# Performance work log

Hardware: AMD Instinct MI355X
Metric: run time of the kernel (lower is better)

Reference implementation:

```python
import jax, jax.numpy as jnp
import numpy as np

EPS = 1e-5

def conv1d(x, w, b, stride, pad):
    # x: [N, Cin, L], w: [Cout, Cin, K]
    out = jax.lax.conv_general_dilated(x, w, (stride,), [(pad, pad)], dimension_numbers=('NCH', 'OIH', 'NCH'))
    return out + b[None, :, None]

def bn_eval(x, g, b):
    # BatchNorm1d in eval mode with running_mean=0, running_var=1
    return x * (g / jnp.sqrt(1.0 + EPS))[None, :, None] + b[None, :, None]

def maxpool3(x):
    return jax.lax.reduce_window(x, -jnp.inf, jax.lax.max, (1, 1, 3), (1, 1, 3), 'VALID')

def layer_norm(x, g, b):
    m = x.mean(-1, keepdims=True)
    v = ((x - m) ** 2).mean(-1, keepdims=True)
    return (x - m) / jnp.sqrt(v + EPS) * g + b

def lstm_dir(x, w_ih, w_hh, b_ih, b_hh, reverse):
    # x: [B, S, I]; torch gate order i, f, g, o
    B = x.shape[0]; H = w_hh.shape[1]
    xs = jnp.einsum('bsi,gi->bsg', x, w_ih) + b_ih + b_hh
    if reverse:
        xs = xs[:, ::-1]
    def step(carry, xt):
        h, c = carry
        gates = xt + h @ w_hh.T
        i, f, g, o = jnp.split(gates, 4, axis=-1)
        c = jax.nn.sigmoid(f) * c + jax.nn.sigmoid(i) * jnp.tanh(g)
        h = jax.nn.sigmoid(o) * jnp.tanh(c)
        return (h, c), h
    init = (jnp.zeros((B, H), x.dtype), jnp.zeros((B, H), x.dtype))
    _, hs = jax.lax.scan(step, init, jnp.swapaxes(xs, 0, 1))
    hs = jnp.swapaxes(hs, 0, 1)
    return hs[:, ::-1] if reverse else hs

def setup_inputs() -> dict:
    key = jax.random.key(0)
    ks = iter(jax.random.split(key, 48))
    def rn(shape, s=0.05):
        return jax.random.normal(next(ks), shape, jnp.float32) * s
    B, S, C, T, F0, Hg, Hl, NC = 64, 20, 8, 3000, 64, 128, 256, 5
    return dict(
        x=jax.random.normal(next(ks), (B, S, C, T), jnp.float32),
        edge_index=jax.random.randint(next(ks), (2, 56), 0, C, jnp.int32),
        conv1_w=rn((16, 1, 7)), conv1_b=jnp.zeros(16), bn1_g=jnp.ones(16), bn1_b=jnp.zeros(16),
        conv2_w=rn((32, 16, 5)), conv2_b=jnp.zeros(32), bn2_g=jnp.ones(32), bn2_b=jnp.zeros(32),
        conv3_w=rn((F0, 32, 3)), conv3_b=jnp.zeros(F0), bn3_g=jnp.ones(F0), bn3_b=jnp.zeros(F0),
        gcn0_w=rn((Hg, F0)), gcn0_b=jnp.zeros(Hg),
        gcn1_w=rn((Hg, Hg)), gcn1_b=jnp.zeros(Hg),
        gnn_ln_g=jnp.ones(Hg), gnn_ln_b=jnp.zeros(Hg),
        w_ih_l0=rn((4 * Hl, Hg)), w_hh_l0=rn((4 * Hl, Hl)), b_ih_l0=jnp.zeros(4 * Hl), b_hh_l0=jnp.zeros(4 * Hl),
        w_ih_l0r=rn((4 * Hl, Hg)), w_hh_l0r=rn((4 * Hl, Hl)), b_ih_l0r=jnp.zeros(4 * Hl), b_hh_l0r=jnp.zeros(4 * Hl),
        w_ih_l1=rn((4 * Hl, 2 * Hl)), w_hh_l1=rn((4 * Hl, Hl)), b_ih_l1=jnp.zeros(4 * Hl), b_hh_l1=jnp.zeros(4 * Hl),
        w_ih_l1r=rn((4 * Hl, 2 * Hl)), w_hh_l1r=rn((4 * Hl, Hl)), b_ih_l1r=jnp.zeros(4 * Hl), b_hh_l1r=jnp.zeros(4 * Hl),
        lstm_ln_g=jnp.ones(2 * Hl), lstm_ln_b=jnp.zeros(2 * Hl),
        cls_w=rn((NC, 2 * Hl)), cls_b=jnp.zeros(NC),
    )

def reference(x, edge_index, conv1_w, conv1_b, bn1_g, bn1_b, conv2_w, conv2_b, bn2_g, bn2_b, conv3_w, conv3_b, bn3_g, bn3_b, gcn0_w, gcn0_b, gcn1_w, gcn1_b, gnn_ln_g, gnn_ln_b, w_ih_l0, w_hh_l0, b_ih_l0, b_hh_l0, w_ih_l0r, w_hh_l0r, b_ih_l0r, b_hh_l0r, w_ih_l1, w_hh_l1, b_ih_l1, b_hh_l1, w_ih_l1r, w_hh_l1r, b_ih_l1r, b_hh_l1r, lstm_ln_g, lstm_ln_b, cls_w, cls_b):
    B, S, C, T = x.shape
    # batched per-channel CNN over all B*S epochs at once (original: python double loop)
    h = x.reshape(B * S * C, 1, T)
    h = maxpool3(jax.nn.relu(bn_eval(conv1d(h, conv1_w, conv1_b, 2, 3), bn1_g, bn1_b)))
    h = maxpool3(jax.nn.relu(bn_eval(conv1d(h, conv2_w, conv2_b, 2, 2), bn2_g, bn2_b)))
    h = jax.nn.relu(bn_eval(conv1d(h, conv3_w, conv3_b, 1, 1), bn3_g, bn3_b))
    feats = h.mean(-1).reshape(B * S, C, -1)  # AdaptiveAvgPool1d(1) -> [BS, C, 64]
    # GCNConv normalized adjacency: D^-1/2 (A + I) D^-1/2, graph is tiny (C nodes) so dense is exact and efficient
    src, dst = edge_index[0], edge_index[1]
    A = jnp.zeros((C, C), x.dtype).at[dst, src].add(1.0) + jnp.eye(C, dtype=x.dtype)
    dinv = 1.0 / jnp.sqrt(A.sum(1))
    An = A * dinv[:, None] * dinv[None, :]
    g1 = jax.nn.relu(jnp.einsum('ij,bjf->bif', An, feats @ gcn0_w.T) + gcn0_b)  # dropout off (eval)
    g2 = jnp.einsum('ij,bjf->bif', An, g1 @ gcn1_w.T) + gcn1_b
    g2 = layer_norm(g2, gnn_ln_g, gnn_ln_b)
    emb = g2.mean(1).reshape(B, S, -1)  # mean over nodes -> [B, S, 128]
    l0 = jnp.concatenate([lstm_dir(emb, w_ih_l0, w_hh_l0, b_ih_l0, b_hh_l0, False),
                          lstm_dir(emb, w_ih_l0r, w_hh_l0r, b_ih_l0r, b_hh_l0r, True)], -1)
    l1 = jnp.concatenate([lstm_dir(l0, w_ih_l1, w_hh_l1, b_ih_l1, b_hh_l1, False),
                          lstm_dir(l0, w_ih_l1r, w_hh_l1r, b_ih_l1r, b_hh_l1r, True)], -1)
    out = layer_norm(l1, lstm_ln_g, lstm_ln_b)
    return out @ cls_w.T + cls_b  # [B, S, 5]
```

## Files before the change

### kernel.cpp

```cpp
#include <hip/hip_runtime.h>
#include <hip/hip_bf16.h>

#define DEVI __device__ __forceinline__

typedef _Float16 h2f16 __attribute__((ext_vector_type(2)));
typedef _Float16 f16x4 __attribute__((ext_vector_type(4)));
typedef _Float16 f16x8 __attribute__((ext_vector_type(8)));
typedef float    f32x4 __attribute__((ext_vector_type(4)));
union U4H { uint4 u; h2f16 h[4]; };
union F8  { f16x8 v8; f16x4 v4[2]; };

DEVI float sigf(float x){ return 1.f/(1.f + __expf(-x)); }
DEVI float tanh_f(float x){
  float ax = fabsf(x);
  float e = __expf(-2.f*ax);
  float t = (1.f - e)/(1.f + e);
  return copysignf(t, x);
}
DEVI h2f16 hmax2(h2f16 a, h2f16 b){
  h2f16 r; r[0] = a[0] > b[0] ? a[0] : b[0]; r[1] = a[1] > b[1] ? a[1] : b[1]; return r;
}

__global__ __launch_bounds__(256) void k_prep(
  const int* __restrict__ ei, float* __restrict__ An,
  const float* __restrict__ w2, const float* __restrict__ w3,
  const float* __restrict__ bg2, const float* __restrict__ bg3,
  _Float16* __restrict__ bw2f, _Float16* __restrict__ bw3f,
  const float* __restrict__ a0, const float* __restrict__ a1,
  const float* __restrict__ a2, const float* __restrict__ a3,
  const float* __restrict__ a4, const float* __restrict__ a5,
  _Float16* __restrict__ o0, _Float16* __restrict__ o1,
  _Float16* __restrict__ o2, _Float16* __restrict__ o3,
  _Float16* __restrict__ o4, _Float16* __restrict__ o5,
  const float* __restrict__ whh0, const float* __restrict__ whh0r,
  const float* __restrict__ whh1, const float* __restrict__ whh1r,
  h2f16* __restrict__ wt0f, h2f16* __restrict__ wt0r,
  h2f16* __restrict__ wt1f, h2f16* __restrict__ wt1r)
{
  const int bid = blockIdx.x, tid = threadIdx.x;
  if (bid == 0){
    __shared__ float A[64];
    __shared__ float dinv[8];
    if (tid<64) A[tid] = ((tid>>3)==(tid&7)) ? 1.f : 0.f;
    __syncthreads();
    if (tid==0){
      for (int e=0;e<56;e++){ int s=ei[e], d=ei[56+e]; A[d*8+s] += 1.f; }
    }
    __syncthreads();
    if (tid<8){ float s=0.f; for (int j=0;j<8;j++) s+=A[tid*8+j]; dinv[tid]=rsqrtf(s); }
    __syncthreads();
    if (tid<64) An[tid] = A[tid]*dinv[tid>>3]*dinv[tid&7];
    return;
  }
  if (bid <= 24){
    const int i = (bid-1)*256 + tid;
    const float rs = rsqrtf(1.f+1e-5f);
    if (i < 3072){
      const int j = i&7, m = (i>>3)&15, g = (i>>7)&3, nt = (i>>9)&1, s = i>>10;
      const int kk = 32*s + 8*g + j;
      const int k = kk >> 4, ic = kk & 15, oc = nt*16 + m;
      bw2f[i] = (_Float16)((k < 5 ? w2[oc*80 + ic*5 + k] : 0.f) * (bg2[oc]*rs));
    }
    if (i < 6144){
      const int j = i&7, m = (i>>3)&15, g = (i>>7)&3, wv = (i>>9)&3, s = i>>11;
      const int kk = 32*s + 8*g + j;
      const int k = kk >> 5, ic = kk & 31, oc = wv*16 + m;
      bw3f[i] = (_Float16)(w3[oc*96 + ic*3 + k] * (bg3[oc]*rs));
    }
    return;
  }
  if (bid <= 5240){
    const int i = (bid-25)*256 + tid;
    if      (i <  131072) o0[i] = (_Float16)a0[i];
    else if (i <  262144) o1[i-131072] = (_Float16)a1[i-131072];
    else if (i <  786432) o2[i-262144] = (_Float16)a2[i-262144];
    else if (i < 1310720) o3[i-786432] = (_Float16)a3[i-786432];
    else if (i < 1318912) o4[i-1310720] = (_Float16)a4[i-1310720];
    else if (i < 1335296) o5[i-1318912] = (_Float16)a5[i-1318912];
    return;
  }
  {
    const int idx = (bid-5241)*256 + tid;
    const int which = idx >> 17, i = idx & 131071;
    const int g = i & 1023, jp = i >> 10;
    const float* in = (which==0) ? whh0 : (which==1) ? whh0r : (which==2) ? whh1 : whh1r;
    h2f16* outp    = (which==0) ? wt0f : (which==1) ? wt0r  : (which==2) ? wt1f : wt1r;
    h2f16 p;
    p[0] = (_Float16)in[g*256 + 2*jp];
    p[1] = (_Float16)in[g*256 + 2*jp + 1];
    outp[(long)jp*1024 + g] = p;
  }
}

__global__ __launch_bounds__(512,8) void k_conv(
    const float* __restrict__ x,
    const float* __restrict__ w1g, const float* __restrict__ c1b,
    const float* __restrict__ bg1, const float* __restrict__ bb1,
    const _Float16* __restrict__ bw2f,
    const float* __restrict__ c2b, const float* __restrict__ bg2, const float* __restrict__ bb2,
    const _Float16* __restrict__ bw3f,
    const float* __restrict__ c3b, const float* __restrict__ bg3, const float* __restrict__ bb3,
    _Float16* __restrict__ feats)
{
  __shared__ __align__(16) unsigned char smb[38592];
  __shared__ h2f16 w1p[16][4];
  __shared__ float kb1o[16], kb2o[32], kb3o[64];
  __shared__ float redc[8][16];
  h2f16* sxh = reinterpret_cast<h2f16*>(smb + 20160);
  const int tid = threadIdx.x;
  const long sig = blockIdx.x;
  const float* xg = x + sig*3000;

  {
    const float4* xg4 = reinterpret_cast<const float4*>(xg);
    for (int i=tid; i<750; i+=512){
      float4 v = xg4[i];
      h2f16 p0; p0[0]=(_Float16)v.x; p0[1]=(_Float16)v.y;
      h2f16 p1; p1[0]=(_Float16)v.z; p1[1]=(_Float16)v.w;
      sxh[2*i+2] = p0; sxh[2*i+3] = p1;
    }
    if (tid<3){
      h2f16 z; z[0]=(_Float16)0.f; z[1]=(_Float16)0.f;
      sxh[tid<2 ? tid : 1502] = z;
    }
    if (tid<32){
      const int rr = tid>>3, cp = tid&7;
      const int row = (rr<2) ? rr : (500+rr);
      h2f16 z; z[0]=(_Float16)0.f; z[1]=(_Float16)0.f;
      *reinterpret_cast<h2f16*>(smb + row*40 + 4*cp) = z;
    }
    const float rs = rsqrtf(1.f+1e-5f);
    if (tid<64){
      const int c = tid>>2, j = tid&3;
      const float s = bg1[c]*rs;
      h2f16 p;
      if (j==0){ p[0]=(_Float16)0.f; p[1]=(_Float16)(w1g[c*7+0]*s); }
      else     { p[0]=(_Float16)(w1g[c*7+2*j-1]*s); p[1]=(_Float16)(w1g[c*7+2*j]*s); }
      w1p[c][j] = p;
    }
    if (tid<16) kb1o[tid] = c1b[tid]*(bg1[tid]*rs) + bb1[tid];
    if (tid<32) kb2o[tid] = c2b[tid]*(bg2[tid]*rs) + bb2[tid];
    if (tid<64) kb3o[tid] = c3b[tid]*(bg3[tid]*rs) + bb3[tid];
  }
  __syncthreads();

  {
    const int cp = tid & 7;
    h2f16 wpa[4], wpb[4];
    #pragma unroll
    for (int j=0;j<4;j++){ wpa[j] = w1p[2*cp][j]; wpb[j] = w1p[2*cp+1][j]; }
    const float oa = kb1o[2*cp], ob = kb1o[2*cp+1];
    for (int u = tid>>3; u<500; u+=64){
      h2f16 xq[6];
      #pragma unroll
      for (int r=0;r<6;r++) xq[r] = sxh[3*u + r];
      float a0=0.f,a1=0.f,a2=0.f,b0=0.f,b1=0.f,b2=0.f;
      #pragma unroll
      for (int j=0;j<4;j++){
        a0 = __builtin_amdgcn_fdot2(xq[j],   wpa[j], a0, false);
        a1 = __builtin_amdgcn_fdot2(xq[j+1], wpa[j], a1, false);
        a2 = __builtin_amdgcn_fdot2(xq[j+2], wpa[j], a2, false);
        b0 = __builtin_amdgcn_fdot2(xq[j],   wpb[j], b0, false);
        b1 = __builtin_amdgcn_fdot2(xq[j+1], wpb[j], b1, false);
        b2 = __builtin_amdgcn_fdot2(xq[j+2], wpb[j], b2, false);
      }
      const float ya = fmaxf(fmaxf(fmaxf(a0,a1),a2) + oa, 0.f);
      const float yb = fmaxf(fmaxf(fmaxf(b0,b1),b2) + ob, 0.f);
      h2f16 p; p[0]=(_Float16)ya; p[1]=(_Float16)yb;
      *reinterpret_cast<h2f16*>(smb + (u+2)*40 + 4*cp) = p;
    }
  }
  __syncthreads();

  const int wv = tid >> 6, lane = tid & 63;
  const int m = lane & 15, g = lane >> 4;

  {
    const int nt = wv & 1;
    f16x8 bf[3];
    #pragma unroll
    for (int s=0;s<3;s++)
      bf[s] = *reinterpret_cast<const f16x8*>(&bw2f[(((s*2+nt)*4+g)*16+m)*8]);
    const int oc = nt*16 + m;
    const float of = kb2o[oc];
    #pragma unroll
    for (int i=0;i<4;i++){
      const int mt = (wv>>1) + 4*i;
      const int trow = mt*16 + m;
      f32x4 acc = {0.f,0.f,0.f,0.f};
      #pragma unroll
      for (int s=0;s<3;s++){
        const int kk = 32*s + 8*g;
        const int k = kk >> 4;
        const int ab = 80*trow + 40*k + 16*(g&1);
        F8 a;
        a.v4[0] = *reinterpret_cast<const f16x4*>(smb + ab);
        a.v4[1] = *reinterpret_cast<const f16x4*>(smb + ab + 8);
        acc = __builtin_amdgcn_mfma_f32_16x16x32_f16(a.v8, bf[s], acc, 0,0,0);
      }
      #pragma unroll
      for (int r=0;r<4;r++){
        const int t = mt*16 + 4*g + r;
        const float z = fmaxf(acc[r] + of, 0.f);
        *reinterpret_cast<_Float16*>(smb + 20160 + t*72 + 2*oc) = (_Float16)z;
      }
    }
  }
  __syncthreads();

  {
    if (tid < 240){
      const int rr = tid >> 4, cc = tid & 15;
      const int row = (rr == 0) ? 0 : (83 + rr);
      h2f16 z; z[0]=(_Float16)0.f; z[1]=(_Float16)0.f;
      *reinterpret_cast<h2f16*>(smb + row*80 + 4*cc) = z;
    }
    for (int i=tid; i<1328; i+=512){
      const int u = i >> 4, cc = i & 15;
      h2f16 a = *reinterpret_cast<const h2f16*>(smb + 20160 + (3*u)*72 + 4*cc);
      h2f16 b = *reinterpret_cast<const h2f16*>(smb + 20160 + (3*u+1)*72 + 4*cc);
      h2f16 c = *reinterpret_cast<const h2f16*>(smb + 20160 + (3*u+2)*72 + 4*cc);
      *reinterpret_cast<h2f16*>(smb + (u+1)*80 + 4*cc) = hmax2(hmax2(a,b), c);
    }
  }
  __syncthreads();

  {
    const int nt = wv & 3;
    f16x8 bf[3];
    #pragma unroll
    for (int s=0;s<3;s++)
      bf[s] = *reinterpret_cast<const f16x8*>(&bw3f[(((s*4+nt)*4+g)*16+m)*8]);
    const int oc = nt*16 + m;
    const float of = kb3o[oc];
    float macc = 0.f;
    #pragma unroll
    for (int q=0;q<3;q++){
      const int mt = (wv>>2) + 2*q;
      const int trow = mt*16 + m;
      f32x4 acc = {0.f,0.f,0.f,0.f};
      #pragma unroll
      for (int s=0;s<3;s++){
        f16x8 af = *reinterpret_cast<const f16x8*>(smb + (trow + s)*80 + 16*g);
        acc = __builtin_amdgcn_mfma_f32_16x16x32_f16(af, bf[s], acc, 0,0,0);
      }
      #pragma unroll
      for (int r=0;r<4;r++){
        const int t = mt*16 + 4*g + r;
        if (t < 83) macc += fmaxf(acc[r] + of, 0.f);
      }
    }
    macc += __shfl_xor(macc, 16);
    macc += __shfl_xor(macc, 32);
    if (lane < 16) redc[wv][m] = macc;
  }
  __syncthreads();
  if (tid < 64)
    feats[sig*64 + tid] = (_Float16)((redc[tid>>4][tid&15] + redc[(tid>>4)+4][tid&15]) * (1.f/83.f));
}

__global__ __launch_bounds__(256) void k_gemm_mf(
  const _Float16* __restrict__ X, const _Float16* __restrict__ W,
  const float* __restrict__ b1, const float* __restrict__ b2,
  float* __restrict__ C, int M, int N, int K, int ldc)
{
  __shared__ __align__(16) unsigned char lds[128*72];
  unsigned char* Xs = lds;
  unsigned char* Ws = lds + 64*72;
  const int tid = threadIdx.x;
  const int m0 = blockIdx.y*64, n0 = blockIdx.x*64;
  const int wv = tid>>6, lane = tid&63, m = lane&15, g = lane>>4;
  const int sr = tid>>2, sq = tid&3;
  f32x4 acc[4] = {{0.f,0.f,0.f,0.f},{0.f,0.f,0.f,0.f},{0.f,0.f,0.f,0.f},{0.f,0.f,0.f,0.f}};
  for (int k0=0; k0<K; k0+=32){
    uint4 xa = *reinterpret_cast<const uint4*>(X + (long)(m0+sr)*K + k0 + sq*8);
    uint4 wa = *reinterpret_cast<const uint4*>(W + (long)(n0+sr)*K + k0 + sq*8);
    __syncthreads();
    *reinterpret_cast<uint4*>(Xs + sr*72 + sq*16) = xa;
    *reinterpret_cast<uint4*>(Ws + sr*72 + sq*16) = wa;
    __syncthreads();
    f16x8 af = *reinterpret_cast<const f16x8*>(Xs + (wv*16+m)*72 + g*16);
    #pragma unroll
    for (int nt=0;nt<4;nt++){
      f16x8 bf = *reinterpret_cast<const f16x8*>(Ws + (nt*16+m)*72 + g*16);
      acc[nt] = __builtin_amdgcn_mfma_f32_16x16x32_f16(af, bf, acc[nt], 0,0,0);
    }
  }
  #pragma unroll
  for (int nt=0;nt<4;nt++){
    const int col = n0 + nt*16 + m;
    float bias = 0.f;
    if (b1) bias += b1[col];
    if (b2) bias += b2[col];
    #pragma unroll
    for (int r=0;r<4;r++)
      C[(long)(m0 + wv*16 + g*4 + r)*ldc + col] = acc[nt][r] + bias;
  }
}

__global__ __launch_bounds__(256) void k_gemm_mf2(
  const _Float16* __restrict__ X,
  const _Float16* __restrict__ Wa, const _Float16* __restrict__ Wb,
  const float* __restrict__ b1a, const float* __restrict__ b2a,
  const float* __restrict__ b1b, const float* __restrict__ b2b,
  float* __restrict__ C, int co, int M, int N, int K, int ldc)
{
  __shared__ __align__(16) unsigned char lds[128*72];
  unsigned char* Xs = lds;
  unsigned char* Ws = lds + 64*72;
  const int z = blockIdx.z;
  const _Float16* W = z ? Wb : Wa;
  const float* b1 = z ? b1b : b1a;
  const float* b2 = z ? b2b : b2a;
  float* Cz = C + (z ? co : 0);
  const int tid = threadIdx.x;
  const int m0 = blockIdx.y*64, n0 = blockIdx.x*64;
  const int wv = tid>>6, lane = tid&63, m = lane&15, g = lane>>4;
  const int sr = tid>>2, sq = tid&3;
  f32x4 acc[4] = {{0.f,0.f,0.f,0.f},{0.f,0.f,0.f,0.f},{0.f,0.f,0.f,0.f},{0.f,0.f,0.f,0.f}};
  for (int k0=0; k0<K; k0+=32){
    uint4 xa = *reinterpret_cast<const uint4*>(X + (long)(m0+sr)*K + k0 + sq*8);
    uint4 wa = *reinterpret_cast<const uint4*>(W + (long)(n0+sr)*K + k0 + sq*8);
    __syncthreads();
    *reinterpret_cast<uint4*>(Xs + sr*72 + sq*16) = xa;
    *reinterpret_cast<uint4*>(Ws + sr*72 + sq*16) = wa;
    __syncthreads();
    f16x8 af = *reinterpret_cast<const f16x8*>(Xs + (wv*16+m)*72 + g*16);
    #pragma unroll
    for (int nt=0;nt<4;nt++){
      f16x8 bf = *reinterpret_cast<const f16x8*>(Ws + (nt*16+m)*72 + g*16);
      acc[nt] = __builtin_amdgcn_mfma_f32_16x16x32_f16(af, bf, acc[nt], 0,0,0);
    }
  }
  #pragma unroll
  for (int nt=0;nt<4;nt++){
    const int col = n0 + nt*16 + m;
    float bias = b1[col] + b2[col];
    #pragma unroll
    for (int r=0;r<4;r++)
      Cz[(long)(m0 + wv*16 + g*4 + r)*ldc + col] = acc[nt][r] + bias;
  }
}

__global__ __launch_bounds__(256) void k_mix1(
  const float* __restrict__ tmp0, const float* __restrict__ An,
  const float* __restrict__ b0, _Float16* __restrict__ g1)
{
  __shared__ float ans[64];
  if (threadIdx.x < 64) ans[threadIdx.x] = An[threadIdx.x];
  __syncthreads();
  const long idx = (long)blockIdx.x*256 + threadIdx.x;
  const int g = (int)(idx >> 7), j = (int)(idx & 127);
  const float* base = tmp0 + (long)g*1024;
  float t[8];
  #pragma unroll
  for (int c=0;c<8;c++) t[c] = base[c*128+j];
  const float bj = b0[j];
  #pragma unroll
  for (int i=0;i<8;i++){
    float s = bj;
    #pragma unroll
    for (int c=0;c<8;c++) s += ans[i*8+c]*t[c];
    g1[(long)g*1024 + i*128 + j] = (_Float16)fmaxf(s, 0.f);
  }
}

__global__ __launch_bounds__(128) void k_mix2(
  const float* __restrict__ tmp1, const float* __restrict__ An,
  const float* __restrict__ b1, const float* __restrict__ lng,
  const float* __restrict__ lnb, _Float16* __restrict__ emb)
{
  const int g = blockIdx.x, j = threadIdx.x;
  __shared__ float ans[64];
  __shared__ float g2s[8*128];
  __shared__ float stats[16];
  if (j<64) ans[j] = An[j];
  const float* base = tmp1 + (long)g*1024;
  float t[8];
  #pragma unroll
  for (int c=0;c<8;c++) t[c] = base[c*128 + j];
  const float bj = b1[j];
  __syncthreads();
  #pragma unroll
  for (int i=0;i<8;i++){
    float s = bj;
    #pragma unroll
    for (int c=0;c<8;c++) s += ans[i*8+c]*t[c];
    g2s[i*128+j] = s;
  }
  __syncthreads();
  {
    const int c = j>>4, l = j&15;
    float s=0.f, sq=0.f;
    for (int jj=l; jj<128; jj+=16){ float v=g2s[c*128+jj]; s+=v; sq+=v*v; }
    #pragma unroll
    for (int off=8; off>=1; off>>=1){ s += __shfl_xor(s, off); sq += __shfl_xor(sq, off); }
    if (l==0){
      float m = s*(1.f/128.f);
      stats[2*c] = m;
      stats[2*c+1] = rsqrtf(sq*(1.f/128.f) - m*m + 1e-5f);
    }
  }
  __syncthreads();
  float acc=0.f;
  #pragma unroll
  for (int i=0;i<8;i++) acc += (g2s[i*128+j] - stats[2*i]) * stats[2*i+1];
  emb[(long)g*128 + j] = (_Float16)(lng[j]*acc*0.125f + lnb[j]);
}

__global__ __launch_bounds__(1024) void k_lstm(
    const float* __restrict__ xs,
    const h2f16* __restrict__ wtf,
    const h2f16* __restrict__ wtr,
    float* __restrict__ outf,
    _Float16* __restrict__ outh)
{
  const int S = 20;
  const int b = blockIdx.x >> 1, dir = blockIdx.x & 1;
  const h2f16* wt = dir ? wtr : wtf;
  __shared__ float part[4][1024];
  __shared__ _Float16 hsh[256];
  __shared__ __align__(16) unsigned char wlds[98304];
  const int tid = threadIdx.x;
  const int jg = tid >> 8, r = tid & 255, grow = r*4;
  uint4 wreg[20];
  #pragma unroll
  for (int jp=0;jp<20;jp++)
    wreg[jp] = *reinterpret_cast<const uint4*>(
        reinterpret_cast<const unsigned int*>(wt + (long)(jg*32+jp)*1024 + grow));
  {
    const uint4* wsrc = reinterpret_cast<const uint4*>(wt);
    uint4* wdst = reinterpret_cast<uint4*>(wlds);
    for (int i=tid; i<6144; i+=1024){
      const int src = (i < 3072) ? (5120 + i) : (13312 + (i - 3072));
      wdst[i] = wsrc[src];
    }
  }
  if (tid < 256) hsh[tid] = (_Float16)0.f;
  float cc = 0.f;
  __syncthreads();
  const h2f16* hp2 = reinterpret_cast<const h2f16*>(hsh);
  for (int st=0; st<S; ++st){
    const int t = dir ? (S-1-st) : st;
    float a0=0.f,a1=0.f,a2=0.f,a3=0.f;
    #pragma unroll
    for (int jp=0; jp<20; ++jp){
      const h2f16 hv = hp2[jg*32 + jp];
      U4H w; w.u = wreg[jp];
      a0 = __builtin_amdgcn_fdot2(hv, w.h[0], a0, false);
      a1 = __builtin_amdgcn_fdot2(hv, w.h[1], a1, false);
      a2 = __builtin_amdgcn_fdot2(hv, w.h[2], a2, false);
      a3 = __builtin_amdgcn_fdot2(hv, w.h[3], a3, false);
    }
    if (jg < 2){
      #pragma unroll 6
      for (int jp=20; jp<32; ++jp){
        const h2f16 hv = hp2[jg*32 + jp];
        U4H w; w.u = *reinterpret_cast<const uint4*>(
            wlds + (long)(jg*12 + (jp-20))*4096 + grow*4);
        a0 = __builtin_amdgcn_fdot2(hv, w.h[0], a0, false);
        a1 = __builtin_amdgcn_fdot2(hv, w.h[1], a1, false);
        a2 = __builtin_amdgcn_fdot2(hv, w.h[2], a2, false);
        a3 = __builtin_amdgcn_fdot2(hv, w.h[3], a3, false);
      }
    } else {
      #pragma unroll 6
      for (int jp=20; jp<32; ++jp){
        const h2f16 hv = hp2[jg*32 + jp];
        U4H w; w.u = *reinterpret_cast<const uint4*>(
            reinterpret_cast<const unsigned int*>(wt + (long)(jg*32+jp)*1024 + grow));
        a0 = __builtin_amdgcn_fdot2(hv, w.h[0], a0, false);
        a1 = __builtin_amdgcn_fdot2(hv, w.h[1], a1, false);
        a2 = __builtin_amdgcn_fdot2(hv, w.h[2], a2, false);
        a3 = __builtin_amdgcn_fdot2(hv, w.h[3], a3, false);
      }
    }
    *reinterpret_cast<float4*>(&part[jg][grow]) = make_float4(a0,a1,a2,a3);
    __syncthreads();
    if (tid < 256){
      const float* xrow = xs + ((long)b*S + t)*2048 + dir*1024;
      float g0 = xrow[tid]
               + (part[0][tid]      + part[1][tid])      + (part[2][tid]      + part[3][tid]);
      float g1 = xrow[256+tid]
               + (part[0][256+tid]  + part[1][256+tid])  + (part[2][256+tid]  + part[3][256+tid]);
      float g2 = xrow[512+tid]
               + (part[0][512+tid]  + part[1][512+tid])  + (part[2][512+tid]  + part[3][512+tid]);
      float g3 = xrow[768+tid]
               + (part[0][768+tid]  + part[1][768+tid])  + (part[2][768+tid]  + part[3][768+tid]);
      cc = sigf(g1)*cc + sigf(g0)*tanh_f(g2);
      const float h = sigf(g3)*tanh_f(cc);
      hsh[tid] = (_Float16)h;
      const long o = ((long)b*S + t)*512 + dir*256 + tid;
      if (outf) outf[o] = h;
      if (outh) outh[o] = (_Float16)h;
    }
    __syncthreads();
  }
}

__global__ __launch_bounds__(128) void k_lncls(
  const float* __restrict__ in, const float* __restrict__ g,
  const float* __restrict__ b, const float* __restrict__ cw,
  const float* __restrict__ cb, float* __restrict__ out)
{
  const int row = blockIdx.x, tid = threadIdx.x;
  __shared__ float sred[4];
  __shared__ float cred[2][5];
  float4 v = *reinterpret_cast<const float4*>(in + (long)row*512 + tid*4);
  float s  = v.x+v.y+v.z+v.w;
  float sq = v.x*v.x+v.y*v.y+v.z*v.z+v.w*v.w;
  #pragma unroll
  for (int off=32; off>=1; off>>=1){ s += __shfl_xor(s, off); sq += __shfl_xor(sq, off); }
  const int wv = tid>>6;
  if ((tid&63)==0){ sred[wv*2]=s; sred[wv*2+1]=sq; }
  __syncthreads();
  const float S = sred[0]+sred[2], SQ = sred[1]+sred[3];
  const float m = S*(1.f/512.f);
  const float rstd = rsqrtf(SQ*(1.f/512.f) - m*m + 1e-5f);
  float4 gg = *reinterpret_cast<const float4*>(g + tid*4);
  float4 bb = *reinterpret_cast<const float4*>(b + tid*4);
  const float n0 = (v.x-m)*rstd*gg.x + bb.x;
  const float n1 = (v.y-m)*rstd*gg.y + bb.y;
  const float n2 = (v.z-m)*rstd*gg.z + bb.z;
  const float n3 = (v.w-m)*rstd*gg.w + bb.w;
  #pragma unroll
  for (int nc=0; nc<5; ++nc){
    float4 w = *reinterpret_cast<const float4*>(cw + nc*512 + tid*4);
    float p = n0*w.x + n1*w.y + n2*w.z + n3*w.w;
    #pragma unroll
    for (int off=32; off>=1; off>>=1) p += __shfl_xor(p, off);
    if ((tid&63)==0) cred[wv][nc] = p;
  }
  __syncthreads();
  if (tid < 5) out[(long)row*5 + tid] = cred[0][tid] + cred[1][tid] + cb[tid];
}

extern "C" void kernel_launch(void* const* d_in, const int* in_sizes, int n_in,
                              void* d_out, int out_size, void* d_ws, size_t ws_size,
                              hipStream_t stream)
{
  const float* x     = (const float*)d_in[0];
  const int*   ei    = (const int*)d_in[1];
  const float* w1    = (const float*)d_in[2];
  const float* c1b   = (const float*)d_in[3];
  const float* bg1   = (const float*)d_in[4];
  const float* bb1   = (const float*)d_in[5];
  const float* w2    = (const float*)d_in[6];
  const float* c2b   = (const float*)d_in[7];
  const float* bg2   = (const float*)d_in[8];
  const float* bb2   = (const float*)d_in[9];
  const float* w3    = (const float*)d_in[10];
  const float* c3b   = (const float*)d_in[11];
  const float* bg3   = (const float*)d_in[12];
  const float* bb3   = (const float*)d_in[13];
  const float* gcn0w = (const float*)d_in[14];
  const float* gcn0b = (const float*)d_in[15];
  const float* gcn1w = (const float*)d_in[16];
  const float* gcn1b = (const float*)d_in[17];
  const float* lng   = (const float*)d_in[18];
  const float* lnb   = (const float*)d_in[19];
  const float* wih0  = (const float*)d_in[20];
  const float* whh0  = (const float*)d_in[21];
  const float* bih0  = (const float*)d_in[22];
  const float* bhh0  = (const float*)d_in[23];
  const float* wih0r = (const float*)d_in[24];
  const float* whh0r = (const float*)d_in[25];
  const float* bih0r = (const float*)d_in[26];
  const float* bhh0r = (const float*)d_in[27];
  const float* wih1  = (const float*)d_in[28];
  const float* whh1  = (const float*)d_in[29];
  const float* bih1  = (const float*)d_in[30];
  const float* bhh1  = (const float*)d_in[31];
  const float* wih1r = (const float*)d_in[32];
  const float* whh1r = (const float*)d_in[33];
  const float* bih1r = (const float*)d_in[34];
  const float* bhh1r = (const float*)d_in[35];
  const float* lstmg = (const float*)d_in[36];
  const float* lstmb = (const float*)d_in[37];
  const float* clsw  = (const float*)d_in[38];
  const float* clsb  = (const float*)d_in[39];
  float* ws  = (float*)d_ws;
  float* out = (float*)d_out;

  float*    An      = ws + 0;
  _Float16* bw2f    = (_Float16*)(ws + 64);
  _Float16* bw3f    = (_Float16*)(ws + 1600);
  _Float16* feats16 = (_Float16*)(ws + 4672);
  _Float16* g1b16   = (_Float16*)(ws + 332352);
  _Float16* emb16   = (_Float16*)(ws + 987712);
  _Float16* l0h     = (_Float16*)(ws + 1069632);
  _Float16* w0f     = (_Float16*)(ws + 1397312);
  _Float16* w0rf    = (_Float16*)(ws + 1462848);
  _Float16* w1f     = (_Float16*)(ws + 1528384);
  _Float16* w1rf    = (_Float16*)(ws + 1790528);
  _Float16* gw0f    = (_Float16*)(ws + 2052672);
  _Float16* gw1f    = (_Float16*)(ws + 2056768);
  h2f16*    wt0f    = (h2f16*)(ws + 2064960);
  h2f16*    wt0r    = (h2f16*)(ws + 2196032);
  h2f16*    wt1f    = (h2f16*)(ws + 2327104);
  h2f16*    wt1r    = (h2f16*)(ws + 2458176);
  float*    l1f     = ws + 2589248;
  float*    xs      = ws + 3244608;
  float*    tmp     = xs;

  k_prep<<<7289, 256, 0, stream>>>(ei, An, w2, w3, bg2, bg3, bw2f, bw3f,
                                   wih0, wih0r, wih1, wih1r, gcn0w, gcn1w,
                                   w0f, w0rf, w1f, w1rf, gw0f, gw1f,
                                   whh0, whh0r, whh1, whh1r,
                                   wt0f, wt0r, wt1f, wt1r);
  k_conv<<<10240, 512, 0, stream>>>(x, w1,c1b,bg1,bb1, bw2f,c2b,bg2,bb2,
                                    bw3f,c3b,bg3,bb3, feats16);

  k_gemm_mf<<<dim3(2, 160), 256, 0, stream>>>(feats16, gw0f, nullptr, nullptr, tmp, 10240, 128, 64, 128);
  k_mix1<<<640,256,0,stream>>>(tmp, An, gcn0b, g1b16);
  k_gemm_mf<<<dim3(2, 160), 256, 0, stream>>>(g1b16, gw1f, nullptr, nullptr, tmp, 10240, 128, 128, 128);
  k_mix2<<<1280,128,0,stream>>>(tmp, An, gcn1b, lng, lnb, emb16);

  k_gemm_mf2<<<dim3(16, 20, 2), 256, 0, stream>>>(emb16, w0f, w0rf,
      bih0, bhh0, bih0r, bhh0r, xs, 1024, 1280, 1024, 128, 2048);
  k_lstm<<<128, 1024, 0, stream>>>(xs, wt0f, wt0r, nullptr, l0h);

  k_gemm_mf2<<<dim3(16, 20, 2), 256, 0, stream>>>(l0h, w1f, w1rf,
      bih1, bhh1, bih1r, bhh1r, xs, 1024, 1280, 1024, 512, 2048);
  k_lstm<<<128, 1024, 0, stream>>>(xs, wt1f, wt1r, l1f, nullptr);

  k_lncls<<<1280, 128, 0, stream>>>(l1f, lstmg, lstmb, clsw, clsb, out);
}
```

Before: 326.8 us.

## Fuse GCN GEMMs with adjacency mixing and layernorm; shift LSTM weights to LDS

Merges each GCN linear GEMM with its neighbouring step: adjacency mixing plus ReLU for the first layer, and adjacency mixing plus layernorm plus node mean for the second. Results are staged in LDS, so the fp32 intermediate no longer goes through global memory and two kernel launches disappear. Separately, the LSTM kernel keeps 16 weight rows per thread in registers instead of 20 and puts more of the recurrent weight in LDS (128 KB). This lowers register pressure but raises LDS use and LDS load traffic in the recurrent loop.

After: 293.1 us. 10.3% less time.

```diff
diff --git a/kernel.cpp b/kernel.cpp
--- a/kernel.cpp
+++ b/kernel.cpp
@@ -259,18 +259,21 @@
     feats[sig*64 + tid] = (_Float16)((redc[tid>>4][tid&15] + redc[(tid>>4)+4][tid&15]) * (1.f/83.f));
 }
 
-__global__ __launch_bounds__(256) void k_gemm_mf(
+__global__ __launch_bounds__(256) void k_gcn1(
   const _Float16* __restrict__ X, const _Float16* __restrict__ W,
-  const float* __restrict__ b1, const float* __restrict__ b2,
-  float* __restrict__ C, int M, int N, int K, int ldc)
-{
-  __shared__ __align__(16) unsigned char lds[128*72];
+  const float* __restrict__ An, const float* __restrict__ b0,
+  _Float16* __restrict__ g1, int K)
+{
+  __shared__ __align__(16) unsigned char lds[17408];
+  __shared__ float ans[64];
   unsigned char* Xs = lds;
-  unsigned char* Ws = lds + 64*72;
+  unsigned char* Ws = lds + 4608;
+  float* Cs = reinterpret_cast<float*>(lds);
   const int tid = threadIdx.x;
   const int m0 = blockIdx.y*64, n0 = blockIdx.x*64;
   const int wv = tid>>6, lane = tid&63, m = lane&15, g = lane>>4;
   const int sr = tid>>2, sq = tid&3;
+  if (tid<64) ans[tid] = An[tid];
   f32x4 acc[4] = {{0.f,0.f,0.f,0.f},{0.f,0.f,0.f,0.f},{0.f,0.f,0.f,0.f},{0.f,0.f,0.f,0.f}};
   for (int k0=0; k0<K; k0+=32){
     uint4 xa = *reinterpret_cast<const uint4*>(X + (long)(m0+sr)*K + k0 + sq*8);
@@ -286,15 +289,107 @@
       acc[nt] = __builtin_amdgcn_mfma_f32_16x16x32_f16(af, bf, acc[nt], 0,0,0);
     }
   }
+  __syncthreads();
   #pragma unroll
-  for (int nt=0;nt<4;nt++){
-    const int col = n0 + nt*16 + m;
-    float bias = 0.f;
-    if (b1) bias += b1[col];
-    if (b2) bias += b2[col];
+  for (int nt=0;nt<4;nt++)
     #pragma unroll
     for (int r=0;r<4;r++)
-      C[(long)(m0 + wv*16 + g*4 + r)*ldc + col] = acc[nt][r] + bias;
+      Cs[(wv*16 + g*4 + r)*68 + nt*16 + m] = acc[nt][r];
+  __syncthreads();
+  for (int idx=tid; idx<512; idx+=256){
+    const int gg = idx>>6, j = idx&63;
+    float t[8];
+    #pragma unroll
+    for (int c=0;c<8;c++) t[c] = Cs[(gg*8+c)*68 + j];
+    const float bj = b0[n0+j];
+    #pragma unroll
+    for (int i=0;i<8;i++){
+      float s = bj;
+      #pragma unroll
+      for (int c=0;c<8;c++) s += ans[i*8+c]*t[c];
+      g1[(long)(m0 + gg*8 + i)*128 + n0 + j] = (_Float16)fmaxf(s, 0.f);
+    }
+  }
+}
+
+__global__ __launch_bounds__(256) void k_gcn2(
+  const _Float16* __restrict__ X, const _Float16* __restrict__ W,
+  const float* __restrict__ An, const float* __restrict__ b1,
+  const float* __restrict__ lng, const float* __restrict__ lnb,
+  _Float16* __restrict__ emb)
+{
+  __shared__ __align__(16) unsigned char lds[33792];
+  __shared__ float ans[64];
+  unsigned char* Xs = lds;
+  unsigned char* Ws = lds + 4608;
+  float* Cs = reinterpret_cast<float*>(lds);
+  const int tid = threadIdx.x;
+  const int m0 = blockIdx.x*64;
+  const int wv = tid>>6, lane = tid&63, m = lane&15, g = lane>>4;
+  const int sr = tid>>2, sq = tid&3;
+  if (tid<64) ans[tid] = An[tid];
+  f32x4 acc[8] = {};
+  for (int k0=0; k0<128; k0+=32){
+    uint4 xa = *reinterpret_cast<const uint4*>(X + (long)(m0+sr)*128 + k0 + sq*8);
+    uint4 wa0 = *reinterpret_cast<const uint4*>(W + (long)(tid>>1)*128 + k0 + (tid&1)*16);
+    uint4 wa1 = *reinterpret_cast<const uint4*>(W + (long)(tid>>1)*128 + k0 + (tid&1)*16 + 8);
+    __syncthreads();
+    *reinterpret_cast<uint4*>(Xs + sr*72 + sq*16) = xa;
+    *reinterpret_cast<uint4*>(Ws + (tid>>1)*72 + (tid&1)*32) = wa0;
+    *reinterpret_cast<uint4*>(Ws + (tid>>1)*72 + (tid&1)*32 + 16) = wa1;
+    __syncthreads();
+    f16x8 af = *reinterpret_cast<const f16x8*>(Xs + (wv*16+m)*72 + g*16);
+    #pragma unroll
+    for (int nt=0;nt<8;nt++){
+      f16x8 bf = *reinterpret_cast<const f16x8*>(Ws + (nt*16+m)*72 + g*16);
+      acc[nt] = __builtin_amdgcn_mfma_f32_16x16x32_f16(af, bf, acc[nt], 0,0,0);
+    }
+  }
+  __syncthreads();
+  #pragma unroll
+  for (int nt=0;nt<8;nt++)
+    #pragma unroll
+    for (int r=0;r<4;r++)
+      Cs[(wv*16 + g*4 + r)*132 + nt*16 + m] = acc[nt][r];
+  __syncthreads();
+  {
+    const int s = tid>>5, l = tid&31;
+    float g2v[8][4];
+    #pragma unroll
+    for (int jj=0;jj<4;jj++){
+      const int j = l + jj*32;
+      float t[8];
+      #pragma unroll
+      for (int c=0;c<8;c++) t[c] = Cs[(s*8+c)*132 + j];
+      const float bj = b1[j];
+      #pragma unroll
+      for (int i=0;i<8;i++){
+        float v = bj;
+        #pragma unroll
+        for (int c=0;c<8;c++) v += ans[i*8+c]*t[c];
+        g2v[i][jj] = v;
+      }
+    }
+    float mi[8], ri[8];
+    #pragma unroll
+    for (int i=0;i<8;i++){
+      float sm=0.f, sq2=0.f;
+      #pragma unroll
+      for (int jj=0;jj<4;jj++){ sm += g2v[i][jj]; sq2 += g2v[i][jj]*g2v[i][jj]; }
+      #pragma unroll
+      for (int off=16; off>=1; off>>=1){ sm += __shfl_xor(sm, off); sq2 += __shfl_xor(sq2, off); }
+      const float mu = sm*(1.f/128.f);
+      mi[i] = mu;
+      ri[i] = rsqrtf(sq2*(1.f/128.f) - mu*mu + 1e-5f);
+    }
+    #pragma unroll
+    for (int jj=0;jj<4;jj++){
+      const int j = l + jj*32;
+      float a = 0.f;
+      #pragma unroll
+      for (int i=0;i<8;i++) a += (g2v[i][jj]-mi[i])*ri[i];
+      emb[(long)(blockIdx.x*8 + s)*128 + j] = (_Float16)(lng[j]*a*0.125f + lnb[j]);
+    }
   }
 }
 
@@ -342,72 +437,6 @@
   }
 }
 
-__global__ __launch_bounds__(256) void k_mix1(
-  const float* __restrict__ tmp0, const float* __restrict__ An,
-  const float* __restrict__ b0, _Float16* __restrict__ g1)
-{
-  __shared__ float ans[64];
-  if (threadIdx.x < 64) ans[threadIdx.x] = An[threadIdx.x];
-  __syncthreads();
-  const long idx = (long)blockIdx.x*256 + threadIdx.x;
-  const int g = (int)(idx >> 7), j = (int)(idx & 127);
-  const float* base = tmp0 + (long)g*1024;
-  float t[8];
-  #pragma unroll
-  for (int c=0;c<8;c++) t[c] = base[c*128+j];
-  const float bj = b0[j];
-  #pragma unroll
-  for (int i=0;i<8;i++){
-    float s = bj;
-    #pragma unroll
-    for (int c=0;c<8;c++) s += ans[i*8+c]*t[c];
-    g1[(long)g*1024 + i*128 + j] = (_Float16)fmaxf(s, 0.f);
-  }
-}
-
-__global__ __launch_bounds__(128) void k_mix2(
-  const float* __restrict__ tmp1, const float* __restrict__ An,
-  const float* __restrict__ b1, const float* __restrict__ lng,
-  const float* __restrict__ lnb, _Float16* __restrict__ emb)
-{
-  const int g = blockIdx.x, j = threadIdx.x;
-  __shared__ float ans[64];
-  __shared__ float g2s[8*128];
-  __shared__ float stats[16];
-  if (j<64) ans[j] = An[j];
-  const float* base = tmp1 + (long)g*1024;
-  float t[8];
-  #pragma unroll
-  for (int c=0;c<8;c++) t[c] = base[c*128 + j];
-  const float bj = b1[j];
-  __syncthreads();
-  #pragma unroll
-  for (int i=0;i<8;i++){
-    float s = bj;
-    #pragma unroll
-    for (int c=0;c<8;c++) s += ans[i*8+c]*t[c];
-    g2s[i*128+j] = s;
-  }
-  __syncthreads();
-  {
-    const int c = j>>4, l = j&15;
-    float s=0.f, sq=0.f;
-    for (int jj=l; jj<128; jj+=16){ float v=g2s[c*128+jj]; s+=v; sq+=v*v; }
-    #pragma unroll
-    for (int off=8; off>=1; off>>=1){ s += __shfl_xor(s, off); sq += __shfl_xor(sq, off); }
-    if (l==0){
-      float m = s*(1.f/128.f);
-      stats[2*c] = m;
-      stats[2*c+1] = rsqrtf(sq*(1.f/128.f) - m*m + 1e-5f);
-    }
-  }
-  __syncthreads();
-  float acc=0.f;
-  #pragma unroll
-  for (int i=0;i<8;i++) acc += (g2s[i*128+j] - stats[2*i]) * stats[2*i+1];
-  emb[(long)g*128 + j] = (_Float16)(lng[j]*acc*0.125f + lnb[j]);
-}
-
 __global__ __launch_bounds__(1024) void k_lstm(
     const float* __restrict__ xs,
     const h2f16* __restrict__ wtf,
@@ -420,19 +449,19 @@
   const h2f16* wt = dir ? wtr : wtf;
   __shared__ float part[4][1024];
   __shared__ _Float16 hsh[256];
-  __shared__ __align__(16) unsigned char wlds[98304];
+  __shared__ __align__(16) unsigned char wlds[131072];
   const int tid = threadIdx.x;
   const int jg = tid >> 8, r = tid & 255, grow = r*4;
-  uint4 wreg[20];
+  uint4 wreg[16];
   #pragma unroll
-  for (int jp=0;jp<20;jp++)
+  for (int jp=0;jp<16;jp++)
     wreg[jp] = *reinterpret_cast<const uint4*>(
         reinterpret_cast<const unsigned int*>(wt + (long)(jg*32+jp)*1024 + grow));
   {
     const uint4* wsrc = reinterpret_cast<const uint4*>(wt);
     uint4* wdst = reinterpret_cast<uint4*>(wlds);
-    for (int i=tid; i<6144; i+=1024){
-      const int src = (i < 3072) ? (5120 + i) : (13312 + (i - 3072));
+    for (int i=tid; i<8192; i+=1024){
+      const int src = (i < 4096) ? (4096 + i) : (12288 + (i - 4096));
       wdst[i] = wsrc[src];
     }
   }
@@ -444,7 +473,7 @@
     const int t = dir ? (S-1-st) : st;
     float a0=0.f,a1=0.f,a2=0.f,a3=0.f;
     #pragma unroll
-    for (int jp=0; jp<20; ++jp){
+    for (int jp=0; jp<16; ++jp){
       const h2f16 hv = hp2[jg*32 + jp];
       U4H w; w.u = wreg[jp];
       a0 = __builtin_amdgcn_fdot2(hv, w.h[0], a0, false);
@@ -453,19 +482,19 @@
       a3 = __builtin_amdgcn_fdot2(hv, w.h[3], a3, false);
     }
     if (jg < 2){
-      #pragma unroll 6
-      for (int jp=20; jp<32; ++jp){
+      #pragma unroll 8
+      for (int jp=16; jp<32; ++jp){
         const h2f16 hv = hp2[jg*32 + jp];
         U4H w; w.u = *reinterpret_cast<const uint4*>(
-            wlds + (long)(jg*12 + (jp-20))*4096 + grow*4);
+            wlds + (long)(jg*16 + (jp-16))*4096 + grow*4);
         a0 = __builtin_amdgcn_fdot2(hv, w.h[0], a0, false);
         a1 = __builtin_amdgcn_fdot2(hv, w.h[1], a1, false);
         a2 = __builtin_amdgcn_fdot2(hv, w.h[2], a2, false);
         a3 = __builtin_amdgcn_fdot2(hv, w.h[3], a3, false);
       }
     } else {
-      #pragma unroll 6
-      for (int jp=20; jp<32; ++jp){
+      #pragma unroll 8
+      for (int jp=16; jp<32; ++jp){
         const h2f16 hv = hp2[jg*32 + jp];
         U4H w; w.u = *reinterpret_cast<const uint4*>(
             reinterpret_cast<const unsigned int*>(wt + (long)(jg*32+jp)*1024 + grow));
@@ -601,7 +630,6 @@
   h2f16*    wt1r    = (h2f16*)(ws + 2458176);
   float*    l1f     = ws + 2589248;
   float*    xs      = ws + 3244608;
-  float*    tmp     = xs;
 
   k_prep<<<7289, 256, 0, stream>>>(ei, An, w2, w3, bg2, bg3, bw2f, bw3f,
                                    wih0, wih0r, wih1, wih1r, gcn0w, gcn1w,
@@ -611,10 +639,8 @@
   k_conv<<<10240, 512, 0, stream>>>(x, w1,c1b,bg1,bb1, bw2f,c2b,bg2,bb2,
                                     bw3f,c3b,bg3,bb3, feats16);
 
-  k_gemm_mf<<<dim3(2, 160), 256, 0, stream>>>(feats16, gw0f, nullptr, nullptr, tmp, 10240, 128, 64, 128);
-  k_mix1<<<640,256,0,stream>>>(tmp, An, gcn0b, g1b16);
-  k_gemm_mf<<<dim3(2, 160), 256, 0, stream>>>(g1b16, gw1f, nullptr, nullptr, tmp, 10240, 128, 128, 128);
-  k_mix2<<<1280,128,0,stream>>>(tmp, An, gcn1b, lng, lnb, emb16);
+  k_gcn1<<<dim3(2, 160), 256, 0, stream>>>(feats16, gw0f, An, gcn0b, g1b16, 64);
+  k_gcn2<<<160, 256, 0, stream>>>(g1b16, gw1f, An, gcn1b, lng, lnb, emb16);
 
   k_gemm_mf2<<<dim3(16, 20, 2), 256, 0, stream>>>(emb16, w0f, w0rf,
       bih0, bhh0, bih0r, bhh0r, xs, 1024, 1280, 1024, 128, 2048);
```
